# Kernel tuning notes

Hardware: AMD Instinct MI355X
Metric: run time of the kernel (lower is better)

## Reference

```python
import jax, jax.numpy as jnp
import numpy as np

C = 256      # channels (multiple of 32 for GroupNorm)
K = 3        # kernel
PAD = 1      # padding
G = 32       # GroupNorm groups
EPS = 1e-5


def setup_inputs() -> dict:
    key = jax.random.key(0)
    ks = jax.random.split(key, 7)
    B, H, W = 4, 64, 64
    return {
        "x": jax.random.normal(ks[0], (B, C, H, W), jnp.float32),
        "offset": jax.random.normal(ks[1], (B, 2 * K * K, H, W), jnp.float32),
        "weight": jax.random.normal(ks[2], (C, C, K, K), jnp.float32) * 0.01,
        "att_w": jax.random.normal(ks[3], (1, C), jnp.float32) * 0.01,
        "att_b": jnp.zeros((1,), jnp.float32),
        "gamma": jnp.ones((C,), jnp.float32),
        "beta": jnp.zeros((C,), jnp.float32),
    }


def _bilinear_one(xb, py, px):
    # xb: [C, H, W]; py, px: [KK, H, W] fractional sample coords (zero-pad outside)
    H, W = xb.shape[1], xb.shape[2]
    y0 = jnp.floor(py)
    x0 = jnp.floor(px)
    y1 = y0 + 1.0
    x1 = x0 + 1.0
    wy1 = py - y0
    wy0 = 1.0 - wy1
    wx1 = px - x0
    wx0 = 1.0 - wx1

    def g(yi, xi):
        valid = (yi >= 0) & (yi < H) & (xi >= 0) & (xi < W)
        yc = jnp.clip(yi, 0, H - 1).astype(jnp.int32)
        xc = jnp.clip(xi, 0, W - 1).astype(jnp.int32)
        return xb[:, yc, xc] * valid[None].astype(xb.dtype)  # [C, KK, H, W]

    return (g(y0, x0) * (wy0 * wx0)[None] + g(y0, x1) * (wy0 * wx1)[None]
            + g(y1, x0) * (wy1 * wx0)[None] + g(y1, x1) * (wy1 * wx1)[None])


def reference(x, offset, weight, att_w, att_b, gamma, beta):
    B, Cc, H, W = x.shape
    KK = K * K
    off = offset.reshape(B, KK, 2, H, W)  # (dy, dx) per kernel tap
    ii, jj = jnp.meshgrid(jnp.arange(K), jnp.arange(K), indexing='ij')
    dky = (ii - PAD).reshape(KK).astype(x.dtype)
    dkx = (jj - PAD).reshape(KK).astype(x.dtype)
    ys = jnp.arange(H, dtype=x.dtype)
    xs = jnp.arange(W, dtype=x.dtype)
    # sample coords [B, KK, H, W]
    py = ys[None, :, None] + dky[:, None, None] + off[:, :, 0]
    px = xs[None, None, :] + dkx[:, None, None] + off[:, :, 1]

    # deformable unfold: [B, C, KK, H, W]
    xu = jax.vmap(_bilinear_one)(x, py, px)

    # max over kernel taps -> channel attention gate
    xm = xu.max(axis=2)  # [B, C, H, W]
    att = jax.nn.sigmoid(jnp.einsum('bchw,oc->bohw', xm, att_w)
                         + att_b[None, :, None, None])  # [B, 1, H, W]

    # gate the unfolded samples, then emulate the conv as one GEMM
    xw = xu * att[:, :, None]  # broadcast over C, KK
    cols = xw.transpose(1, 2, 0, 3, 4).reshape(Cc * KK, B * H * W)  # [C*KK, BHW]
    out = (weight.reshape(Cc, Cc * KK) @ cols).reshape(Cc, B, H, W).transpose(1, 0, 2, 3)

    # GroupNorm(32, C) + ReLU
    og = out.reshape(B, G, Cc // G, H, W)
    mu = og.mean(axis=(2, 3, 4), keepdims=True)
    var = og.var(axis=(2, 3, 4), keepdims=True)
    on = ((og - mu) * jax.lax.rsqrt(var + EPS)).reshape(B, Cc, H, W)
    return jax.nn.relu(on * gamma[None, :, None, None] + beta[None, :, None, None])
```

## Files before the change

### kernel.cpp

```cpp
#include <hip/hip_runtime.h>

#define CT 256
#define KDIM 2304
#define ROUNDS 8
#define COLP 296

typedef unsigned short u16;
typedef __attribute__((ext_vector_type(8))) short bf16x8;
typedef __attribute__((ext_vector_type(4))) float f32x4;

__device__ __forceinline__ unsigned f2b(float f) {
    unsigned u = __float_as_uint(f);
    u += 0x7fffu + ((u >> 16) & 1u);
    return u >> 16;
}
__device__ __forceinline__ float us2f(u16 v) { return __uint_as_float(((unsigned)v) << 16); }
__device__ __forceinline__ float lo_bf(unsigned u) { return __uint_as_float(u << 16); }
__device__ __forceinline__ float hi_bf(unsigned u) { return __uint_as_float(u & 0xffff0000u); }

__global__ __launch_bounds__(256) void k_xprep(const float* __restrict__ x, uint4* __restrict__ xi)
{
    int u = blockIdx.x * 256 + threadIdx.x;
    int bcg = u >> 12, p = u & 4095;
    const float* xp = x + (((size_t)bcg) << 15) + p;
    unsigned r[4];
#pragma unroll
    for (int i = 0; i < 4; ++i) {
        float a = xp[(size_t)(2 * i) << 12];
        float c = xp[(size_t)(2 * i + 1) << 12];
        r[i] = f2b(a) | (f2b(c) << 16);
    }
    uint4 o; o.x = r[0]; o.y = r[1]; o.z = r[2]; o.w = r[3];
    xi[u] = o;
}

__global__ __launch_bounds__(256) void k_wprep(const float* __restrict__ wgt, uint4* __restrict__ pw)
{
    int u = blockIdx.x * 256 + threadIdx.x;
    int kc = u >> 10, rm = u & 1023;
    int m = rm >> 2, j = rm & 3;
    int round = kc / 9, tap = kc - round * 9;
    const float* src = wgt + (size_t)m * KDIM + tap;
    int c0 = round * 32 + j * 8;
    unsigned q[4];
#pragma unroll
    for (int i = 0; i < 4; ++i) {
        float a = src[(size_t)(c0 + 2 * i) * 9];
        float c = src[(size_t)(c0 + 2 * i + 1) * 9];
        q[i] = f2b(a) | (f2b(c) << 16);
    }
    uint4 o; o.x = q[0]; o.y = q[1]; o.z = q[2]; o.w = q[3];
    pw[u] = o;
}

__global__ __launch_bounds__(512, 2) void k_main(const uint4* __restrict__ xi, const float* __restrict__ off,
                                                 const uint4* __restrict__ pw, const float* __restrict__ att_w,
                                                 const float* __restrict__ att_b,
                                                 float* __restrict__ outp, float* __restrict__ gnpart)
{
    __shared__ float4 s_wt[576];
    __shared__ int2 s_off[576];
    __shared__ u16 Xs[7680];
    __shared__ u16 col[64 * COLP];
    __shared__ float s_att[8][64];

    int rowblk = blockIdx.x;
    int b = rowblk >> 6, h = rowblk & 63;
    int tid = threadIdx.x;
    int lane = tid & 63, w = tid >> 6;
    int n = tid & 63, g = tid >> 6;
    int l15 = lane & 15, kb = lane >> 4;
    int wm = w * 32;

    for (int e = tid; e < 576; e += 512) {
        int kk = e >> 6, ww_ = e & 63;
        int ky = kk / 3, kx = kk - ky * 3;
        float dy = off[((size_t)(b * 18 + 2 * kk) * 64 + h) * 64 + ww_];
        float dx = off[((size_t)(b * 18 + 2 * kk + 1) * 64 + h) * 64 + ww_];
        float py = (float)(h + ky - 1) + dy;
        float px = (float)(ww_ + kx - 1) + dx;
        float y0f = floorf(py), x0f = floorf(px);
        int y0 = (int)y0f, x0 = (int)x0f;
        float fy = py - y0f, fx = px - x0f;
        float vy0 = (y0 >= 0 && y0 < 64) ? 1.f : 0.f;
        float vy1 = (y0 >= -1 && y0 < 63) ? 1.f : 0.f;
        float vx0 = (x0 >= 0 && x0 < 64) ? 1.f : 0.f;
        float vx1 = (x0 >= -1 && x0 < 63) ? 1.f : 0.f;
        float4 wt;
        wt.x = (1.f - fy) * (1.f - fx) * vy0 * vx0;
        wt.y = (1.f - fy) * fx * vy0 * vx1;
        wt.z = fy * (1.f - fx) * vy1 * vx0;
        wt.w = fy * fx * vy1 * vx1;
        int yc0 = min(max(y0, 0), 63), yc1 = min(max(y0 + 1, 0), 63);
        int xc0 = min(max(x0, 0), 63), xc1 = min(max(x0 + 1, 0), 63);
        s_wt[e] = wt;
        s_off[e] = make_int2((yc0 * 64 + xc0) | ((yc0 * 64 + xc1) << 16),
                             (yc1 * 64 + xc0) | ((yc1 * 64 + xc1) << 16));
    }

    int r0 = max(0, h - 7), r1 = min(63, h + 7);
    int nrows = r1 - r0 + 1, nw = nrows * 64, rbase = r0 * 64;

    float att_acc = 0.f;
    f32x4 acc[2][4];
#pragma unroll
    for (int mt = 0; mt < 2; ++mt)
#pragma unroll
        for (int nt = 0; nt < 4; ++nt) acc[mt][nt] = (f32x4){0.f, 0.f, 0.f, 0.f};

    for (int round = 0; round < ROUNDS; ++round) {
        for (int sp = 0; sp < 4; ++sp) {
            int cg = round * 4 + sp;
            size_t xibase = (size_t)(b * 32 + cg) << 12;
            __syncthreads();
            for (int u2 = tid; u2 < nrows * 64; u2 += 512)
                ((uint4*)Xs)[u2] = xi[xibase + rbase + u2];
            __syncthreads();
            for (int it = tid; it < 576; it += 512) {
                int tap = it >> 6, nn = it & 63;
                float4 wt = s_wt[it];
                int2 of = s_off[it];
                float wx = wt.x, wy = wt.y, wz = wt.z, ww2 = wt.w;
                int P00 = of.x & 0xffff, P01 = (of.x >> 16) & 0xffff;
                int P10 = of.y & 0xffff, P11 = (of.y >> 16) & 0xffff;
                uint4 c00, c01, c10, c11;
                int Q;
                Q = P00 - rbase;
                if ((unsigned)Q < (unsigned)nw) c00 = *(const uint4*)&Xs[Q * 8]; else c00 = xi[xibase + P00];
                Q = P01 - rbase;
                if ((unsigned)Q < (unsigned)nw) c01 = *(const uint4*)&Xs[Q * 8]; else c01 = xi[xibase + P01];
                Q = P10 - rbase;
                if ((unsigned)Q < (unsigned)nw) c10 = *(const uint4*)&Xs[Q * 8]; else c10 = xi[xibase + P10];
                Q = P11 - rbase;
                if ((unsigned)Q < (unsigned)nw) c11 = *(const uint4*)&Xs[Q * 8]; else c11 = xi[xibase + P11];
                const unsigned* a00 = (const unsigned*)&c00;
                const unsigned* a01 = (const unsigned*)&c01;
                const unsigned* a10 = (const unsigned*)&c10;
                const unsigned* a11 = (const unsigned*)&c11;
                unsigned o[4];
#pragma unroll
                for (int q = 0; q < 4; ++q) {
                    float v0 = wx * lo_bf(a00[q]) + wy * lo_bf(a01[q]) + wz * lo_bf(a10[q]) + ww2 * lo_bf(a11[q]);
                    float v1 = wx * hi_bf(a00[q]) + wy * hi_bf(a01[q]) + wz * hi_bf(a10[q]) + ww2 * hi_bf(a11[q]);
                    o[q] = f2b(v0) | (f2b(v1) << 16);
                }
                uint4 ov; ov.x = o[0]; ov.y = o[1]; ov.z = o[2]; ov.w = o[3];
                *(uint4*)&col[nn * COLP + tap * 32 + sp * 8] = ov;
            }
            __syncthreads();
            {
                int base = n * COLP + sp * 8 + g;
                float mv = us2f(col[base]);
#pragma unroll
                for (int t = 1; t < 9; ++t) mv = fmaxf(mv, us2f(col[base + t * 32]));
                att_acc += att_w[round * 32 + sp * 8 + g] * mv;
            }
        }
        __syncthreads();
#pragma unroll
        for (int ts = 0; ts < 9; ++ts) {
            int kc = round * 9 + ts;
            bf16x8 bf[4];
#pragma unroll
            for (int nt = 0; nt < 4; ++nt)
                bf[nt] = *(const bf16x8*)&col[(nt * 16 + l15) * COLP + ts * 32 + kb * 8];
#pragma unroll
            for (int mt = 0; mt < 2; ++mt) {
                uint4 a = pw[(size_t)kc * 1024 + (wm + mt * 16 + l15) * 4 + kb];
                bf16x8 af = __builtin_bit_cast(bf16x8, a);
#pragma unroll
                for (int nt = 0; nt < 4; ++nt)
                    acc[mt][nt] = __builtin_amdgcn_mfma_f32_16x16x32_bf16(af, bf[nt], acc[mt][nt], 0, 0, 0);
            }
        }
    }

    s_att[g][n] = att_acc;
    __syncthreads();
    if (tid < 64) {
        float s = att_b[0];
#pragma unroll
        for (int q = 0; q < 8; ++q) s += s_att[q][tid];
        s_att[0][tid] = 1.f / (1.f + expf(-s));
    }
    __syncthreads();

    float attn[4];
#pragma unroll
    for (int nt = 0; nt < 4; ++nt) attn[nt] = s_att[0][nt * 16 + l15];

#pragma unroll
    for (int mt = 0; mt < 2; ++mt) {
        float s1 = 0.f, s2 = 0.f;
#pragma unroll
        for (int nt = 0; nt < 4; ++nt)
#pragma unroll
            for (int r = 0; r < 4; ++r) {
                float v = acc[mt][nt][r] * attn[nt];
                int m = wm + mt * 16 + kb * 4 + r;
                outp[(((size_t)(b * CT + m)) << 12) + h * 64 + nt * 16 + l15] = v;
                s1 += v; s2 += v * v;
            }
#pragma unroll
        for (int d = 1; d <= 16; d <<= 1) {
            s1 += __shfl_xor(s1, d);
            s2 += __shfl_xor(s2, d);
        }
        if ((lane & 31) == 0) {
            int gidx = w * 4 + mt * 2 + (kb >> 1);
            gnpart[rowblk * 64 + gidx * 2] = s1;
            gnpart[rowblk * 64 + gidx * 2 + 1] = s2;
        }
    }
}

__global__ __launch_bounds__(128) void k_gnfinal(const float* __restrict__ gnpart, float* __restrict__ stats)
{
    int p = threadIdx.x;
    int bb = p >> 5, gg = p & 31;
    float S1 = 0.f, S2 = 0.f;
    for (int hh = 0; hh < 64; ++hh) {
        S1 += gnpart[(bb * 64 + hh) * 64 + gg * 2];
        S2 += gnpart[(bb * 64 + hh) * 64 + gg * 2 + 1];
    }
    float mean = S1 * (1.f / 32768.f);
    float var = S2 * (1.f / 32768.f) - mean * mean;
    stats[p * 2] = mean;
    stats[p * 2 + 1] = rsqrtf(var + 1e-5f);
}

__global__ __launch_bounds__(256) void k_gnorm(float* __restrict__ outp, const float* __restrict__ stats,
                                               const float* __restrict__ gamma, const float* __restrict__ beta)
{
    int idx = blockIdx.x * 256 + threadIdx.x;
    size_t e = (size_t)idx * 4;
    int c = (int)((e >> 12) & 255);
    int bg = (int)(e >> 15);
    float mean = stats[bg * 2], rstd = stats[bg * 2 + 1];
    float ga = gamma[c], be = beta[c];
    float4 v = ((const float4*)outp)[idx];
    float4 r;
    r.x = fmaxf((v.x - mean) * rstd * ga + be, 0.f);
    r.y = fmaxf((v.y - mean) * rstd * ga + be, 0.f);
    r.z = fmaxf((v.z - mean) * rstd * ga + be, 0.f);
    r.w = fmaxf((v.w - mean) * rstd * ga + be, 0.f);
    ((float4*)outp)[idx] = r;
}

extern "C" void kernel_launch(void* const* d_in, const int* in_sizes, int n_in,
                              void* d_out, int out_size, void* d_ws, size_t ws_size,
                              hipStream_t stream)
{
    const float* x = (const float*)d_in[0];
    const float* off = (const float*)d_in[1];
    const float* wgt = (const float*)d_in[2];
    const float* attw = (const float*)d_in[3];
    const float* attb = (const float*)d_in[4];
    const float* gamma = (const float*)d_in[5];
    const float* beta = (const float*)d_in[6];
    float* outp = (float*)d_out;

    char* ws = (char*)d_ws;
    uint4* xi = (uint4*)ws;
    uint4* pw = (uint4*)(ws + 8388608);
    float* gnpart = (float*)(ws + 9568256);
    float* stats = (float*)(ws + 9633792);

    k_xprep<<<dim3(2048), dim3(256), 0, stream>>>(x, xi);
    k_wprep<<<dim3(288), dim3(256), 0, stream>>>(wgt, pw);
    k_main<<<dim3(256), dim3(512), 0, stream>>>(xi, off, pw, attw, attb, outp, gnpart);
    k_gnfinal<<<dim3(1), dim3(128), 0, stream>>>(gnpart, stats);
    k_gnorm<<<dim3(4096), dim3(256), 0, stream>>>(outp, stats, gamma, beta);
}
```

Measured before the change: 174.8 us.

## Split main kernel into half-row blocks and merge prep and GroupNorm kernels

The main kernel now runs one block per half image row (32 columns), which doubles the grid to 512 blocks so more CUs have work. The attention max-reduction moves out of the per-channel-group loop and runs once per round with vectorized loads, which removes one barrier per sub-step. The two prep kernels are merged into one launch, and the GroupNorm finalize and apply kernels are fused into one per-group kernel, cutting launch count. In exchange, each block does less MFMA work per staged X tile, so the staging of input rows and offsets is repeated across the two halves.

```diff
diff --git a/kernel.cpp b/kernel.cpp
--- a/kernel.cpp
+++ b/kernel.cpp
@@ -14,43 +14,42 @@
     u += 0x7fffu + ((u >> 16) & 1u);
     return u >> 16;
 }
-__device__ __forceinline__ float us2f(u16 v) { return __uint_as_float(((unsigned)v) << 16); }
 __device__ __forceinline__ float lo_bf(unsigned u) { return __uint_as_float(u << 16); }
 __device__ __forceinline__ float hi_bf(unsigned u) { return __uint_as_float(u & 0xffff0000u); }
 
-__global__ __launch_bounds__(256) void k_xprep(const float* __restrict__ x, uint4* __restrict__ xi)
-{
-    int u = blockIdx.x * 256 + threadIdx.x;
-    int bcg = u >> 12, p = u & 4095;
-    const float* xp = x + (((size_t)bcg) << 15) + p;
-    unsigned r[4];
-#pragma unroll
-    for (int i = 0; i < 4; ++i) {
-        float a = xp[(size_t)(2 * i) << 12];
-        float c = xp[(size_t)(2 * i + 1) << 12];
-        r[i] = f2b(a) | (f2b(c) << 16);
-    }
-    uint4 o; o.x = r[0]; o.y = r[1]; o.z = r[2]; o.w = r[3];
-    xi[u] = o;
-}
-
-__global__ __launch_bounds__(256) void k_wprep(const float* __restrict__ wgt, uint4* __restrict__ pw)
-{
-    int u = blockIdx.x * 256 + threadIdx.x;
-    int kc = u >> 10, rm = u & 1023;
-    int m = rm >> 2, j = rm & 3;
-    int round = kc / 9, tap = kc - round * 9;
-    const float* src = wgt + (size_t)m * KDIM + tap;
-    int c0 = round * 32 + j * 8;
-    unsigned q[4];
-#pragma unroll
-    for (int i = 0; i < 4; ++i) {
-        float a = src[(size_t)(c0 + 2 * i) * 9];
-        float c = src[(size_t)(c0 + 2 * i + 1) * 9];
-        q[i] = f2b(a) | (f2b(c) << 16);
-    }
-    uint4 o; o.x = q[0]; o.y = q[1]; o.z = q[2]; o.w = q[3];
-    pw[u] = o;
+__global__ __launch_bounds__(256) void k_prep(const float* __restrict__ x, uint4* __restrict__ xi,
+                                              const float* __restrict__ wgt, uint4* __restrict__ pw)
+{
+    if (blockIdx.x < 2048) {
+        int u = blockIdx.x * 256 + threadIdx.x;
+        int bcg = u >> 12, p = u & 4095;
+        const float* xp = x + (((size_t)bcg) << 15) + p;
+        unsigned r[4];
+#pragma unroll
+        for (int i = 0; i < 4; ++i) {
+            float a = xp[(size_t)(2 * i) << 12];
+            float c = xp[(size_t)(2 * i + 1) << 12];
+            r[i] = f2b(a) | (f2b(c) << 16);
+        }
+        uint4 o; o.x = r[0]; o.y = r[1]; o.z = r[2]; o.w = r[3];
+        xi[u] = o;
+    } else {
+        int u = (blockIdx.x - 2048) * 256 + threadIdx.x;
+        int kc = u >> 10, rm = u & 1023;
+        int m = rm >> 2, j = rm & 3;
+        int round = kc / 9, tap = kc - round * 9;
+        const float* src = wgt + (size_t)m * KDIM + tap;
+        int c0 = round * 32 + j * 8;
+        unsigned q[4];
+#pragma unroll
+        for (int i = 0; i < 4; ++i) {
+            float a = src[(size_t)(c0 + 2 * i) * 9];
+            float c = src[(size_t)(c0 + 2 * i + 1) * 9];
+            q[i] = f2b(a) | (f2b(c) << 16);
+        }
+        uint4 o; o.x = q[0]; o.y = q[1]; o.z = q[2]; o.w = q[3];
+        pw[u] = o;
+    }
 }
 
 __global__ __launch_bounds__(512, 2) void k_main(const uint4* __restrict__ xi, const float* __restrict__ off,
@@ -58,22 +57,22 @@
                                                  const float* __restrict__ att_b,
                                                  float* __restrict__ outp, float* __restrict__ gnpart)
 {
-    __shared__ float4 s_wt[576];
-    __shared__ int2 s_off[576];
+    __shared__ float4 s_wt[288];
+    __shared__ int2 s_off[288];
     __shared__ u16 Xs[7680];
-    __shared__ u16 col[64 * COLP];
-    __shared__ float s_att[8][64];
-
-    int rowblk = blockIdx.x;
-    int b = rowblk >> 6, h = rowblk & 63;
+    __shared__ u16 col[32 * COLP];
+    __shared__ float s_att[32];
+
+    int rowblk = blockIdx.x >> 1, half = blockIdx.x & 1;
+    int b = rowblk >> 6, h = rowblk & 63, n0 = half * 32;
     int tid = threadIdx.x;
     int lane = tid & 63, w = tid >> 6;
-    int n = tid & 63, g = tid >> 6;
     int l15 = lane & 15, kb = lane >> 4;
     int wm = w * 32;
 
-    for (int e = tid; e < 576; e += 512) {
-        int kk = e >> 6, ww_ = e & 63;
+    for (int e = tid; e < 288; e += 512) {
+        int kk = e >> 5, wl = e & 31;
+        int ww_ = n0 + wl;
         int ky = kk / 3, kx = kk - ky * 3;
         float dy = off[((size_t)(b * 18 + 2 * kk) * 64 + h) * 64 + ww_];
         float dx = off[((size_t)(b * 18 + 2 * kk + 1) * 64 + h) * 64 + ww_];
@@ -102,11 +101,11 @@
     int nrows = r1 - r0 + 1, nw = nrows * 64, rbase = r0 * 64;
 
     float att_acc = 0.f;
-    f32x4 acc[2][4];
+    f32x4 acc[2][2];
 #pragma unroll
     for (int mt = 0; mt < 2; ++mt)
 #pragma unroll
-        for (int nt = 0; nt < 4; ++nt) acc[mt][nt] = (f32x4){0.f, 0.f, 0.f, 0.f};
+        for (int nt = 0; nt < 2; ++nt) acc[mt][nt] = (f32x4){0.f, 0.f, 0.f, 0.f};
 
     for (int round = 0; round < ROUNDS; ++round) {
         for (int sp = 0; sp < 4; ++sp) {
@@ -116,11 +115,10 @@
             for (int u2 = tid; u2 < nrows * 64; u2 += 512)
                 ((uint4*)Xs)[u2] = xi[xibase + rbase + u2];
             __syncthreads();
-            for (int it = tid; it < 576; it += 512) {
-                int tap = it >> 6, nn = it & 63;
+            for (int it = tid; it < 288; it += 512) {
+                int tap = it >> 5, nn = it & 31;
                 float4 wt = s_wt[it];
                 int2 of = s_off[it];
-                float wx = wt.x, wy = wt.y, wz = wt.z, ww2 = wt.w;
                 int P00 = of.x & 0xffff, P01 = (of.x >> 16) & 0xffff;
                 int P10 = of.y & 0xffff, P11 = (of.y >> 16) & 0xffff;
                 uint4 c00, c01, c10, c11;
@@ -140,65 +138,71 @@
                 unsigned o[4];
 #pragma unroll
                 for (int q = 0; q < 4; ++q) {
-                    float v0 = wx * lo_bf(a00[q]) + wy * lo_bf(a01[q]) + wz * lo_bf(a10[q]) + ww2 * lo_bf(a11[q]);
-                    float v1 = wx * hi_bf(a00[q]) + wy * hi_bf(a01[q]) + wz * hi_bf(a10[q]) + ww2 * hi_bf(a11[q]);
+                    float v0 = wt.x * lo_bf(a00[q]) + wt.y * lo_bf(a01[q]) + wt.z * lo_bf(a10[q]) + wt.w * lo_bf(a11[q]);
+                    float v1 = wt.x * hi_bf(a00[q]) + wt.y * hi_bf(a01[q]) + wt.z * hi_bf(a10[q]) + wt.w * hi_bf(a11[q]);
                     o[q] = f2b(v0) | (f2b(v1) << 16);
                 }
                 uint4 ov; ov.x = o[0]; ov.y = o[1]; ov.z = o[2]; ov.w = o[3];
                 *(uint4*)&col[nn * COLP + tap * 32 + sp * 8] = ov;
             }
-            __syncthreads();
-            {
-                int base = n * COLP + sp * 8 + g;
-                float mv = us2f(col[base]);
-#pragma unroll
-                for (int t = 1; t < 9; ++t) mv = fmaxf(mv, us2f(col[base + t * 32]));
-                att_acc += att_w[round * 32 + sp * 8 + g] * mv;
-            }
         }
         __syncthreads();
+
+        if (tid < 64) {
+            int nn = tid >> 1, h2 = tid & 1;
+#pragma unroll
+            for (int sp = 0; sp < 4; ++sp) {
+                const u16* base = &col[nn * COLP + sp * 8 + h2 * 4];
+                float m0 = -1e30f, m1 = -1e30f, m2 = -1e30f, m3 = -1e30f;
+#pragma unroll
+                for (int t = 0; t < 9; ++t) {
+                    uint2 v = *(const uint2*)(base + t * 32);
+                    m0 = fmaxf(m0, lo_bf(v.x)); m1 = fmaxf(m1, hi_bf(v.x));
+                    m2 = fmaxf(m2, lo_bf(v.y)); m3 = fmaxf(m3, hi_bf(v.y));
+                }
+                int cb = round * 32 + sp * 8 + h2 * 4;
+                att_acc += att_w[cb] * m0 + att_w[cb + 1] * m1 + att_w[cb + 2] * m2 + att_w[cb + 3] * m3;
+            }
+        }
+
 #pragma unroll
         for (int ts = 0; ts < 9; ++ts) {
             int kc = round * 9 + ts;
-            bf16x8 bf[4];
-#pragma unroll
-            for (int nt = 0; nt < 4; ++nt)
+            bf16x8 bf[2];
+#pragma unroll
+            for (int nt = 0; nt < 2; ++nt)
                 bf[nt] = *(const bf16x8*)&col[(nt * 16 + l15) * COLP + ts * 32 + kb * 8];
 #pragma unroll
             for (int mt = 0; mt < 2; ++mt) {
                 uint4 a = pw[(size_t)kc * 1024 + (wm + mt * 16 + l15) * 4 + kb];
                 bf16x8 af = __builtin_bit_cast(bf16x8, a);
 #pragma unroll
-                for (int nt = 0; nt < 4; ++nt)
+                for (int nt = 0; nt < 2; ++nt)
                     acc[mt][nt] = __builtin_amdgcn_mfma_f32_16x16x32_bf16(af, bf[nt], acc[mt][nt], 0, 0, 0);
             }
         }
     }
 
-    s_att[g][n] = att_acc;
+    if (tid < 64) {
+        float v = att_acc + __shfl_xor(att_acc, 1);
+        if ((tid & 1) == 0) s_att[tid >> 1] = 1.f / (1.f + expf(-(v + att_b[0])));
+    }
     __syncthreads();
-    if (tid < 64) {
-        float s = att_b[0];
-#pragma unroll
-        for (int q = 0; q < 8; ++q) s += s_att[q][tid];
-        s_att[0][tid] = 1.f / (1.f + expf(-s));
-    }
-    __syncthreads();
-
-    float attn[4];
-#pragma unroll
-    for (int nt = 0; nt < 4; ++nt) attn[nt] = s_att[0][nt * 16 + l15];
+
+    float attn[2];
+#pragma unroll
+    for (int nt = 0; nt < 2; ++nt) attn[nt] = s_att[nt * 16 + l15];
 
 #pragma unroll
     for (int mt = 0; mt < 2; ++mt) {
         float s1 = 0.f, s2 = 0.f;
 #pragma unroll
-        for (int nt = 0; nt < 4; ++nt)
+        for (int nt = 0; nt < 2; ++nt)
 #pragma unroll
             for (int r = 0; r < 4; ++r) {
                 float v = acc[mt][nt][r] * attn[nt];
                 int m = wm + mt * 16 + kb * 4 + r;
-                outp[(((size_t)(b * CT + m)) << 12) + h * 64 + nt * 16 + l15] = v;
+                outp[(((size_t)(b * CT + m)) << 12) + h * 64 + n0 + nt * 16 + l15] = v;
                 s1 += v; s2 += v * v;
             }
 #pragma unroll
@@ -208,43 +212,55 @@
         }
         if ((lane & 31) == 0) {
             int gidx = w * 4 + mt * 2 + (kb >> 1);
-            gnpart[rowblk * 64 + gidx * 2] = s1;
-            gnpart[rowblk * 64 + gidx * 2 + 1] = s2;
-        }
-    }
-}
-
-__global__ __launch_bounds__(128) void k_gnfinal(const float* __restrict__ gnpart, float* __restrict__ stats)
-{
-    int p = threadIdx.x;
-    int bb = p >> 5, gg = p & 31;
-    float S1 = 0.f, S2 = 0.f;
-    for (int hh = 0; hh < 64; ++hh) {
-        S1 += gnpart[(bb * 64 + hh) * 64 + gg * 2];
-        S2 += gnpart[(bb * 64 + hh) * 64 + gg * 2 + 1];
-    }
-    float mean = S1 * (1.f / 32768.f);
-    float var = S2 * (1.f / 32768.f) - mean * mean;
-    stats[p * 2] = mean;
-    stats[p * 2 + 1] = rsqrtf(var + 1e-5f);
-}
-
-__global__ __launch_bounds__(256) void k_gnorm(float* __restrict__ outp, const float* __restrict__ stats,
-                                               const float* __restrict__ gamma, const float* __restrict__ beta)
-{
-    int idx = blockIdx.x * 256 + threadIdx.x;
-    size_t e = (size_t)idx * 4;
-    int c = (int)((e >> 12) & 255);
-    int bg = (int)(e >> 15);
-    float mean = stats[bg * 2], rstd = stats[bg * 2 + 1];
-    float ga = gamma[c], be = beta[c];
-    float4 v = ((const float4*)outp)[idx];
-    float4 r;
-    r.x = fmaxf((v.x - mean) * rstd * ga + be, 0.f);
-    r.y = fmaxf((v.y - mean) * rstd * ga + be, 0.f);
-    r.z = fmaxf((v.z - mean) * rstd * ga + be, 0.f);
-    r.w = fmaxf((v.w - mean) * rstd * ga + be, 0.f);
-    ((float4*)outp)[idx] = r;
+            gnpart[blockIdx.x * 64 + gidx * 2] = s1;
+            gnpart[blockIdx.x * 64 + gidx * 2 + 1] = s2;
+        }
+    }
+}
+
+__global__ __launch_bounds__(256) void k_gn(const float* __restrict__ gnpart, const float* __restrict__ gamma,
+                                            const float* __restrict__ beta, float* __restrict__ outp)
+{
+    __shared__ float rs1[128], rs2[128];
+    __shared__ float s_stat[2];
+    int bg = blockIdx.x;
+    int b = bg >> 5, g = bg & 31;
+    int tid = threadIdx.x;
+    if (tid < 128) {
+        int blk = (b * 64 + (tid >> 1)) * 2 + (tid & 1);
+        rs1[tid] = gnpart[blk * 64 + g * 2];
+        rs2[tid] = gnpart[blk * 64 + g * 2 + 1];
+    }
+    __syncthreads();
+    if (tid < 64) {
+        float a = rs1[tid] + rs1[tid + 64];
+        float c = rs2[tid] + rs2[tid + 64];
+#pragma unroll
+        for (int d = 1; d <= 32; d <<= 1) {
+            a += __shfl_xor(a, d);
+            c += __shfl_xor(c, d);
+        }
+        if (tid == 0) {
+            float mean = a * (1.f / 32768.f);
+            float var = c * (1.f / 32768.f) - mean * mean;
+            s_stat[0] = mean;
+            s_stat[1] = rsqrtf(var + 1e-5f);
+        }
+    }
+    __syncthreads();
+    float mean = s_stat[0], rstd = s_stat[1];
+    float4* p4 = (float4*)(outp + ((size_t)(b * CT + g * 8) << 12));
+    for (int i = tid; i < 8192; i += 256) {
+        int c = g * 8 + (i >> 10);
+        float ga = gamma[c], be = beta[c];
+        float4 v = p4[i];
+        float4 r;
+        r.x = fmaxf((v.x - mean) * rstd * ga + be, 0.f);
+        r.y = fmaxf((v.y - mean) * rstd * ga + be, 0.f);
+        r.z = fmaxf((v.z - mean) * rstd * ga + be, 0.f);
+        r.w = fmaxf((v.w - mean) * rstd * ga + be, 0.f);
+        p4[i] = r;
+    }
 }
 
 extern "C" void kernel_launch(void* const* d_in, const int* in_sizes, int n_in,
@@ -264,11 +280,8 @@
     uint4* xi = (uint4*)ws;
     uint4* pw = (uint4*)(ws + 8388608);
     float* gnpart = (float*)(ws + 9568256);
-    float* stats = (float*)(ws + 9633792);
-
-    k_xprep<<<dim3(2048), dim3(256), 0, stream>>>(x, xi);
-    k_wprep<<<dim3(288), dim3(256), 0, stream>>>(wgt, pw);
-    k_main<<<dim3(256), dim3(512), 0, stream>>>(xi, off, pw, attw, attb, outp, gnpart);
-    k_gnfinal<<<dim3(1), dim3(128), 0, stream>>>(gnpart, stats);
-    k_gnorm<<<dim3(4096), dim3(256), 0, stream>>>(outp, stats, gamma, beta);
-}
+
+    k_prep<<<dim3(2336), dim3(256), 0, stream>>>(x, xi, wgt, pw);
+    k_main<<<dim3(512), dim3(512), 0, stream>>>(xi, off, pw, attw, attb, outp, gnpart);
+    k_gn<<<dim3(128), dim3(256), 0, stream>>>(gnpart, gamma, beta, outp);
+}
```

New measurement: 167.2 us. 4.3% less time.
